# Optimization experiments

Measured on AMD Instinct MI355X. Metric: run time of the kernel, lower is better.

## Reference

```python
import jax, jax.numpy as jnp
import numpy as np
from jax import lax

B, h, Ch = 16, 8, 32
HW = 56
N = HW * HW
SPLITS = [64, 96, 96]  # [2*Ch, 3*Ch, 3*Ch] for windows {3,5,7}


def _dwconv(x, w, b, pad):
    # x: [B, C, H, W]; w: [C, 1, k, k] depthwise (feature_group_count=C)
    y = lax.conv_general_dilated(
        x, w, window_strides=(1, 1), padding=[(pad, pad), (pad, pad)],
        feature_group_count=x.shape[1],
        dimension_numbers=('NCHW', 'OIHW', 'NCHW'))
    return y + b[None, :, None, None]


def setup_inputs() -> dict:
    key = jax.random.key(0)
    ks = jax.random.split(key, 6)
    return {
        'q': jax.random.normal(ks[0], (B, h, N, Ch), dtype=jnp.float32),
        'v': jax.random.normal(ks[1], (B, h, N, Ch), dtype=jnp.float32),
        'w3': jax.random.normal(ks[2], (64, 1, 3, 3), dtype=jnp.float32) * 0.1,
        'b3': jnp.zeros((64,), dtype=jnp.float32),
        'w5': jax.random.normal(ks[3], (96, 1, 5, 5), dtype=jnp.float32) * 0.1,
        'b5': jnp.zeros((96,), dtype=jnp.float32),
        'w7': jax.random.normal(ks[4], (96, 1, 7, 7), dtype=jnp.float32) * 0.1,
        'b7': jnp.zeros((96,), dtype=jnp.float32),
        'H': HW,
        'W': HW,
    }


def reference(q, v, w3, b3, w5, b5, w7, b7, H, W):
    # q, v: [B, h, N, Ch]; N == H*W, Nv == N (same-resolution path, no interpolation)
    Bq, hh, Nq, C = q.shape
    # v: B h (H W) Ch -> B (h*Ch) H W
    v_img = jnp.transpose(v, (0, 1, 3, 2)).reshape(Bq, hh * C, H, W)
    v1, v2, v3 = jnp.split(v_img, np.cumsum(SPLITS)[:-1], axis=1)
    conv_v = jnp.concatenate([
        _dwconv(v1, w3, b3, 1),
        _dwconv(v2, w5, b5, 2),
        _dwconv(v3, w7, b7, 3),
    ], axis=1)  # [B, h*Ch, H, W]
    # B (h*Ch) H W -> B h (H W) Ch
    conv_v = conv_v.reshape(Bq, hh, C, H * W).transpose(0, 1, 3, 2)
    ev = q * conv_v  # [B, h, N, Ch]
    # transpose(1,2).flatten(2): [B, N, h*Ch]
    return jnp.transpose(ev, (0, 2, 1, 3)).reshape(Bq, Nq, hh * C)
```

## Files before the change

### kernel.cpp

```cpp
#include <hip/hip_runtime.h>
#include <cstddef>


#define BH 16
#define NH 8
#define CH 32
#define HW 56
#define NN (HW*HW)
#define ROWB (HW*CH*4)
#define RS 58
#define BUF_PX 584
#define BUF_FLOATS (BUF_PX*CH)

typedef float f32x4 __attribute__((ext_vector_type(4)));
typedef unsigned int u32x4 __attribute__((ext_vector_type(4)));

__device__ __forceinline__ f32x4 bload(__amdgpu_buffer_rsrc_t rs, int voff) {
    u32x4 u = __builtin_amdgcn_raw_buffer_load_b128(rs, voff, 0, 0);
    f32x4 f; __builtin_memcpy(&f, &u, 16); return f;
}

template<int K>
__device__ __forceinline__ void run_head(
    const float* __restrict__ q, const float* __restrict__ v,
    const float* __restrict__ w, const float* __restrict__ bias,
    float* __restrict__ out, int b, int hh, int y0, int cbase,
    float* __restrict__ w_lds, float* __restrict__ bufs)
{
    constexpr int P = K / 2;
    constexpr int NR = 7 + K - 1;
    constexpr int NROWS = 4 + 2 * P;
    const int t = threadIdx.x;

    const int nw = K * K * CH;
    for (int i = t; i < nw; i += 256) {
        int tap = i >> 5, c = i & 31;
        w_lds[tap * CH + c] = w[(cbase + c) * (K * K) + tap];
    }

    {
        f32x4 z = {0.f, 0.f, 0.f, 0.f};
        const int NG = P + 2 * NROWS + 1;
        if (t < NG * 8) {
            const int g = t >> 3, sub = t & 7;
            int px;
            if (g < P) px = g;
            else if (g < P + 2 * NROWS) {
                const int rr = (g - P) >> 1;
                px = P + rr * RS + 56 + ((g - P) & 1);
            } else px = P + NROWS * RS;
            *(f32x4*)(bufs + px * CH + sub * 4) = z;
        }
    }

    const int wid  = t >> 6;
    const int lane = t & 63;
    const int y    = y0 + wid;
    const int xseg = lane >> 3;
    const int chq  = lane & 7;
    const int x0   = xseg * 7;
    const int ch   = chq * 4;

    const size_t plane = ((size_t)b * NH + hh) * (size_t)NN * CH;
    const float* vb   = v + plane;
    const float* qrow = q + plane + (size_t)y * (HW * CH);

    f32x4 qf[7];
#pragma unroll
    for (int i = 0; i < 7; ++i)
        qf[i] = *(const f32x4*)(qrow + (size_t)(x0 + i) * CH + ch);

    for (int rr = wid; rr < NROWS; rr += 4) {
        const int yy = y0 - P + rr;
        const bool ok = (unsigned)yy < (unsigned)HW;
        __amdgpu_buffer_rsrc_t rs = __builtin_amdgcn_make_buffer_rsrc(
            (void*)(vb + (ptrdiff_t)yy * (HW * CH)), (short)0, ok ? ROWB : 0, 0x00020000);
        f32x4 ld[7];
#pragma unroll
        for (int k = 0; k < 7; ++k) ld[k] = bload(rs, k * 1024 + lane * 16);
        float* dst = bufs + (size_t)(P + rr * RS) * CH;
#pragma unroll
        for (int k = 0; k < 7; ++k)
            *(f32x4*)(dst + k * 256 + lane * 4) = ld[k];
    }
    __syncthreads();

    const float mL = (xseg == 0) ? 0.f : 1.f;
    const float mR = (xseg == 7) ? 0.f : 1.f;

    const f32x4 bias4 = *(const f32x4*)(bias + cbase + ch);
    f32x4 acc[7];
#pragma unroll
    for (int i = 0; i < 7; ++i) acc[i] = bias4;

#pragma unroll
    for (int dy = 0; dy < K; ++dy) {
        const int rr = wid + dy;
        const float* rb = bufs + (size_t)(rr * RS + x0) * CH + ch;
        f32x4 r[NR];
#pragma unroll
        for (int j = 0; j < NR; ++j)
            r[j] = *(const f32x4*)(rb + j * CH);
        if constexpr (K == 7) { r[0] *= mL; r[NR - 1] *= mR; }

#pragma unroll
        for (int dx = 0; dx < K; ++dx) {
            const f32x4 w4 = *(const f32x4*)(w_lds + (dy * K + dx) * CH + ch);
#pragma unroll
            for (int i = 0; i < 7; ++i)
                acc[i] += r[i + dx] * w4;
        }
    }

    float* obase = out + ((size_t)b * NN + (size_t)y * HW) * (NH * CH) + hh * CH + ch;
#pragma unroll
    for (int i = 0; i < 7; ++i)
        *(f32x4*)(obase + (size_t)(x0 + i) * (NH * CH)) = acc[i] * qf[i];
}

__global__ __launch_bounds__(256, 2)
void clusterformer_fused(const float* __restrict__ q, const float* __restrict__ v,
                         const float* __restrict__ w3, const float* __restrict__ b3,
                         const float* __restrict__ w5, const float* __restrict__ b5,
                         const float* __restrict__ w7, const float* __restrict__ b7,
                         float* __restrict__ out)
{
    __shared__ __align__(16) float bufs[BUF_FLOATS];
    __shared__ __align__(16) float w_lds[49 * CH];

    const int bid  = blockIdx.x;
    const int p_lo = bid & 7;
    const int t2   = bid >> 3;
    const int p_hi = t2 / 14;
    const int yg   = t2 % 14;
    const int p    = p_hi * 8 + p_lo;
    const int b    = p & 15;
    const int hhp  = p >> 4;
    const int hh   = (hhp < 3) ? (5 + hhp) : ((hhp < 6) ? (hhp - 1) : (hhp - 6));
    const int y0   = yg * 4;

    if (hh < 2)      run_head<3>(q, v, w3, b3, out, b, hh, y0, hh * 32,       w_lds, bufs);
    else if (hh < 5) run_head<5>(q, v, w5, b5, out, b, hh, y0, hh * 32 - 64,  w_lds, bufs);
    else             run_head<7>(q, v, w7, b7, out, b, hh, y0, hh * 32 - 160, w_lds, bufs);
}

extern "C" void kernel_launch(void* const* d_in, const int* in_sizes, int n_in,
                              void* d_out, int out_size, void* d_ws, size_t ws_size,
                              hipStream_t stream) {
    const float* q  = (const float*)d_in[0];
    const float* v  = (const float*)d_in[1];
    const float* w3 = (const float*)d_in[2];
    const float* b3 = (const float*)d_in[3];
    const float* w5 = (const float*)d_in[4];
    const float* b5 = (const float*)d_in[5];
    const float* w7 = (const float*)d_in[6];
    const float* b7 = (const float*)d_in[7];
    float* out = (float*)d_out;

    const int grid = BH * NH * 14;
    clusterformer_fused<<<grid, 256, 0, stream>>>(q, v, w3, b3, w5, b5, w7, b7, out);
}
```

Measured before the change: 161.8 us.

## Enlarge row tiles to 14 rows per block with register-blocked multi-row convolution

Each block now handles 14 output rows instead of 4, which cuts the redundant halo loads of v from neighbouring row groups. Each wave register-blocks 3–4 output rows, so every LDS row it loads feeds several accumulators. All of a thread's global row loads are issued before its LDS stores to increase memory-level parallelism, and outputs use nontemporal stores. The cost is a much larger LDS buffer and more registers (launch bounds drop to 1 block per CU), and the grid shrinks to 512 blocks, lowering occupancy and parallelism.

```diff
diff --git a/kernel.cpp b/kernel.cpp
--- a/kernel.cpp
+++ b/kernel.cpp
@@ -9,7 +9,8 @@
 #define NN (HW*HW)
 #define ROWB (HW*CH*4)
 #define RS 58
-#define BUF_PX 584
+#define NROWS_MAX 20
+#define BUF_PX (3 + NROWS_MAX*RS + 1)
 #define BUF_FLOATS (BUF_PX*CH)
 
 typedef float f32x4 __attribute__((ext_vector_type(4)));
@@ -20,6 +21,70 @@
     f32x4 f; __builtin_memcpy(&f, &u, 16); return f;
 }
 
+template<int K, int R>
+__device__ __forceinline__ void conv_rows(
+    const float* __restrict__ q, float* __restrict__ out,
+    const float* __restrict__ bias,
+    int b, int hh, int y0, int sw, int cbase,
+    const float* __restrict__ w_lds, const float* __restrict__ bufs,
+    int lane)
+{
+    constexpr int P  = K / 2;
+    constexpr int NR = 7 + K - 1;
+    const int xseg = lane >> 3;
+    const int chq  = lane & 7;
+    const int x0   = xseg * 7;
+    const int ch   = chq * 4;
+
+    const float mL = (xseg == 0) ? 0.f : 1.f;
+    const float mR = (xseg == 7) ? 0.f : 1.f;
+
+    const f32x4 bias4 = *(const f32x4*)(bias + cbase + ch);
+    f32x4 acc[R][7];
+#pragma unroll
+    for (int u = 0; u < R; ++u)
+#pragma unroll
+        for (int i = 0; i < 7; ++i) acc[u][i] = bias4;
+
+    for (int rr = 0; rr < R + 2 * P; ++rr) {
+        const float* rb = bufs + (size_t)((3 - P + x0) + (sw + rr) * RS) * CH + ch;
+        f32x4 r[NR];
+#pragma unroll
+        for (int j = 0; j < NR; ++j)
+            r[j] = *(const f32x4*)(rb + j * CH);
+        if constexpr (K == 7) { r[0] *= mL; r[NR - 1] *= mR; }
+
+#pragma unroll
+        for (int u = 0; u < R; ++u) {
+            const int dy = rr - u;
+            if ((unsigned)dy < (unsigned)K) {
+#pragma unroll
+                for (int dx = 0; dx < K; ++dx) {
+                    const f32x4 w4 = *(const f32x4*)(w_lds + (dy * K + dx) * CH + ch);
+#pragma unroll
+                    for (int i = 0; i < 7; ++i)
+                        acc[u][i] += r[i + dx] * w4;
+                }
+            }
+        }
+    }
+
+    const size_t plane = ((size_t)b * NH + hh) * (size_t)NN * CH;
+#pragma unroll
+    for (int u = 0; u < R; ++u) {
+        const int y = y0 + sw + u;
+        const float* qrow = q + plane + (size_t)y * (HW * CH);
+        float* obase = out + ((size_t)b * NN + (size_t)y * HW) * (NH * CH) + hh * CH + ch;
+#pragma unroll
+        for (int i = 0; i < 7; ++i) {
+            const int px = x0 + i;
+            const f32x4 q4 = *(const f32x4*)(qrow + (size_t)px * CH + ch);
+            const f32x4 o  = acc[u][i] * q4;
+            __builtin_nontemporal_store(o, (f32x4*)(obase + (size_t)px * (NH * CH)));
+        }
+    }
+}
+
 template<int K>
 __device__ __forceinline__ void run_head(
     const float* __restrict__ q, const float* __restrict__ v,
@@ -28,8 +93,8 @@
     float* __restrict__ w_lds, float* __restrict__ bufs)
 {
     constexpr int P = K / 2;
-    constexpr int NR = 7 + K - 1;
-    constexpr int NROWS = 4 + 2 * P;
+    constexpr int NROWS = 14 + 2 * P;
+    constexpr int NS = (NROWS + 3) / 4;
     const int t = threadIdx.x;
 
     const int nw = K * K * CH;
@@ -40,85 +105,56 @@
 
     {
         f32x4 z = {0.f, 0.f, 0.f, 0.f};
-        const int NG = P + 2 * NROWS + 1;
-        if (t < NG * 8) {
-            const int g = t >> 3, sub = t & 7;
+        const int NG = 3 + 2 * NROWS + 1;
+        for (int i = t; i < NG * 8; i += 256) {
+            const int g = i >> 3, sub = i & 7;
             int px;
-            if (g < P) px = g;
-            else if (g < P + 2 * NROWS) {
-                const int rr = (g - P) >> 1;
-                px = P + rr * RS + 56 + ((g - P) & 1);
-            } else px = P + NROWS * RS;
-            *(f32x4*)(bufs + px * CH + sub * 4) = z;
+            if (g < 3) px = g;
+            else if (g < 3 + 2 * NROWS) {
+                const int s = (g - 3) >> 1;
+                px = 3 + s * RS + 56 + ((g - 3) & 1);
+            } else px = 3 + NROWS * RS;
+            *(f32x4*)(bufs + (size_t)px * CH + sub * 4) = z;
         }
     }
 
     const int wid  = t >> 6;
     const int lane = t & 63;
-    const int y    = y0 + wid;
-    const int xseg = lane >> 3;
-    const int chq  = lane & 7;
-    const int x0   = xseg * 7;
-    const int ch   = chq * 4;
+    const size_t plane = ((size_t)b * NH + hh) * (size_t)NN * CH;
+    const float* vb = v + plane;
 
-    const size_t plane = ((size_t)b * NH + hh) * (size_t)NN * CH;
-    const float* vb   = v + plane;
-    const float* qrow = q + plane + (size_t)y * (HW * CH);
-
-    f32x4 qf[7];
+    f32x4 ld[NS][7];
 #pragma unroll
-    for (int i = 0; i < 7; ++i)
-        qf[i] = *(const f32x4*)(qrow + (size_t)(x0 + i) * CH + ch);
-
-    for (int rr = wid; rr < NROWS; rr += 4) {
-        const int yy = y0 - P + rr;
-        const bool ok = (unsigned)yy < (unsigned)HW;
-        __amdgpu_buffer_rsrc_t rs = __builtin_amdgcn_make_buffer_rsrc(
-            (void*)(vb + (ptrdiff_t)yy * (HW * CH)), (short)0, ok ? ROWB : 0, 0x00020000);
-        f32x4 ld[7];
+    for (int n = 0; n < NS; ++n) {
+        const int s = wid + n * 4;
+        if (s < NROWS) {
+            const int gy = y0 - P + s;
+            const bool ok = (unsigned)gy < (unsigned)HW;
+            __amdgpu_buffer_rsrc_t rs = __builtin_amdgcn_make_buffer_rsrc(
+                (void*)(vb + (ptrdiff_t)gy * (HW * CH)), (short)0, ok ? ROWB : 0, 0x00020000);
 #pragma unroll
-        for (int k = 0; k < 7; ++k) ld[k] = bload(rs, k * 1024 + lane * 16);
-        float* dst = bufs + (size_t)(P + rr * RS) * CH;
+            for (int k = 0; k < 7; ++k) ld[n][k] = bload(rs, k * 1024 + lane * 16);
+        }
+    }
 #pragma unroll
-        for (int k = 0; k < 7; ++k)
-            *(f32x4*)(dst + k * 256 + lane * 4) = ld[k];
+    for (int n = 0; n < NS; ++n) {
+        const int s = wid + n * 4;
+        if (s < NROWS) {
+            float* dst = bufs + (size_t)(3 + s * RS) * CH;
+#pragma unroll
+            for (int k = 0; k < 7; ++k)
+                *(f32x4*)(dst + k * 256 + lane * 4) = ld[n][k];
+        }
     }
     __syncthreads();
 
-    const float mL = (xseg == 0) ? 0.f : 1.f;
-    const float mR = (xseg == 7) ? 0.f : 1.f;
-
-    const f32x4 bias4 = *(const f32x4*)(bias + cbase + ch);
-    f32x4 acc[7];
-#pragma unroll
-    for (int i = 0; i < 7; ++i) acc[i] = bias4;
-
-#pragma unroll
-    for (int dy = 0; dy < K; ++dy) {
-        const int rr = wid + dy;
-        const float* rb = bufs + (size_t)(rr * RS + x0) * CH + ch;
-        f32x4 r[NR];
-#pragma unroll
-        for (int j = 0; j < NR; ++j)
-            r[j] = *(const f32x4*)(rb + j * CH);
-        if constexpr (K == 7) { r[0] *= mL; r[NR - 1] *= mR; }
-
-#pragma unroll
-        for (int dx = 0; dx < K; ++dx) {
-            const f32x4 w4 = *(const f32x4*)(w_lds + (dy * K + dx) * CH + ch);
-#pragma unroll
-            for (int i = 0; i < 7; ++i)
-                acc[i] += r[i + dx] * w4;
-        }
-    }
-
-    float* obase = out + ((size_t)b * NN + (size_t)y * HW) * (NH * CH) + hh * CH + ch;
-#pragma unroll
-    for (int i = 0; i < 7; ++i)
-        *(f32x4*)(obase + (size_t)(x0 + i) * (NH * CH)) = acc[i] * qf[i];
+    if      (wid == 0) conv_rows<K, 4>(q, out, bias, b, hh, y0, 0,  cbase, w_lds, bufs, lane);
+    else if (wid == 1) conv_rows<K, 3>(q, out, bias, b, hh, y0, 4,  cbase, w_lds, bufs, lane);
+    else if (wid == 2) conv_rows<K, 3>(q, out, bias, b, hh, y0, 7,  cbase, w_lds, bufs, lane);
+    else               conv_rows<K, 4>(q, out, bias, b, hh, y0, 10, cbase, w_lds, bufs, lane);
 }
 
-__global__ __launch_bounds__(256, 2)
+__global__ __launch_bounds__(256, 1)
 void clusterformer_fused(const float* __restrict__ q, const float* __restrict__ v,
                          const float* __restrict__ w3, const float* __restrict__ b3,
                          const float* __restrict__ w5, const float* __restrict__ b5,
@@ -131,13 +167,13 @@
     const int bid  = blockIdx.x;
     const int p_lo = bid & 7;
     const int t2   = bid >> 3;
-    const int p_hi = t2 / 14;
-    const int yg   = t2 % 14;
+    const int p_hi = t2 >> 2;
+    const int yg   = t2 & 3;
     const int p    = p_hi * 8 + p_lo;
     const int b    = p & 15;
     const int hhp  = p >> 4;
     const int hh   = (hhp < 3) ? (5 + hhp) : ((hhp < 6) ? (hhp - 1) : (hhp - 6));
-    const int y0   = yg * 4;
+    const int y0   = yg * 14;
 
     if (hh < 2)      run_head<3>(q, v, w3, b3, out, b, hh, y0, hh * 32,       w_lds, bufs);
     else if (hh < 5) run_head<5>(q, v, w5, b5, out, b, hh, y0, hh * 32 - 64,  w_lds, bufs);
@@ -157,6 +193,6 @@
     const float* b7 = (const float*)d_in[7];
     float* out = (float*)d_out;
 
-    const int grid = BH * NH * 14;
+    const int grid = BH * NH * 4;
     clusterformer_fused<<<grid, 256, 0, stream>>>(q, v, w3, b3, w5, b5, w7, b7, out);
 }
```

New measurement: 166.0 us. +2.6%, slower.
